# Performance work log

Measured on AMD Instinct MI355X. Metric: run time of the kernel, lower is better.

## Reference

```python
import jax, jax.numpy as jnp
import numpy as np

H = 1024
V = 32000
L = 15
B = 512


def setup_inputs() -> dict:
    key = jax.random.key(0)
    ks = jax.random.split(key, 16)
    s = 0.02
    return {
        "input_ids": jax.random.randint(ks[0], (B,), 0, V),
        "hidden": jax.random.normal(ks[1], (1, B, H), jnp.float32),
        "encoder_outputs": jax.random.normal(ks[2], (L, B, H), jnp.float32),
        "max_length": L,
        "embedding": jax.random.normal(ks[3], (V, H), jnp.float32) * s,
        "attn1_w": jax.random.normal(ks[4], (1, 2 * H), jnp.float32) * s,
        "attn1_b": jnp.zeros((1,), jnp.float32),
        "combine_w": jax.random.normal(ks[5], (H, 2 * H), jnp.float32) * s,
        "combine_b": jnp.zeros((H,), jnp.float32),
        "w_ih": jax.random.normal(ks[6], (3 * H, H), jnp.float32) * s,
        "w_hh": jax.random.normal(ks[7], (3 * H, H), jnp.float32) * s,
        "b_ih": jnp.zeros((3 * H,), jnp.float32),
        "b_hh": jnp.zeros((3 * H,), jnp.float32),
        "out_w": jax.random.normal(ks[8], (V, H), jnp.float32) * s,
        "out_b": jnp.zeros((V,), jnp.float32),
    }


def reference(input_ids, hidden, encoder_outputs, max_length, embedding,
              attn1_w, attn1_b, combine_w, combine_b,
              w_ih, w_hh, b_ih, b_hh, out_w, out_b):
    # embedding lookup (dropout is identity in eval mode)
    emb = embedding[input_ids]                       # [B, H]
    # Bahdanau-style additive scores: vectorize the per-step python loop
    emb_l = jnp.broadcast_to(emb[None], (max_length, B, H))   # [L, B, H]
    cat = jnp.concatenate([emb_l, encoder_outputs], axis=-1)  # [L, B, 2H]
    scores = cat @ attn1_w.T + attn1_b               # [L, B, 1]
    attn_weights = jax.nn.softmax(scores, axis=0)    # softmax over L
    ctx = jnp.sum(attn_weights * encoder_outputs, axis=0)     # [B, H]
    x = jnp.concatenate([emb, ctx], axis=-1) @ combine_w.T + combine_b  # [B, H]
    # n_layers = 1: relu then one GRU step (seq len 1)
    x = jax.nn.relu(x)
    h = hidden[0]                                    # [B, H]
    gi = x @ w_ih.T + b_ih                           # [B, 3H]
    gh = h @ w_hh.T + b_hh                           # [B, 3H]
    i_r, i_z, i_n = jnp.split(gi, 3, axis=1)
    h_r, h_z, h_n = jnp.split(gh, 3, axis=1)
    r = jax.nn.sigmoid(i_r + h_r)
    z = jax.nn.sigmoid(i_z + h_z)
    n = jnp.tanh(i_n + r * h_n)
    h_new = (1.0 - z) * n + z * h                    # [B, H]
    logits = h_new @ out_w.T + out_b                 # [B, V]
    output = jax.nn.log_softmax(logits, axis=1)
    return output, h_new[None], attn_weights
```

## Files before the change

kernel.cpp:

```cpp
#include <hip/hip_runtime.h>

#define HH 1024
#define VV 32000
#define LL 15
#define BB 512

typedef __bf16 bf16;
typedef __bf16 bf16x4 __attribute__((ext_vector_type(4)));
typedef __bf16 bf16x8 __attribute__((ext_vector_type(8)));
typedef float f32x4 __attribute__((ext_vector_type(4)));

#define VMCNT(n) asm volatile("s_waitcnt vmcnt(" #n ")" ::: "memory")
#define LGKM0    asm volatile("s_waitcnt lgkmcnt(0)" ::: "memory")
#define SBAR     __builtin_amdgcn_s_barrier()
#define SCHED0   __builtin_amdgcn_sched_barrier(0)

__device__ __forceinline__ unsigned short f2bf(float f) {
    unsigned int u = __float_as_uint(f);
    unsigned int r = (u + 0x7fffu + ((u >> 16) & 1u)) >> 16;
    return (unsigned short)r;
}

__device__ __forceinline__ void gld_lds16(const void* g, void* l) {
    __builtin_amdgcn_global_load_lds(
        (const __attribute__((address_space(1))) unsigned int*)g,
        (__attribute__((address_space(3))) unsigned int*)l, 16, 0, 0);
}

__global__ __launch_bounds__(256)
void cvt4_kernel(const float* __restrict__ a0, unsigned short* __restrict__ o0, int n0_,
                 const float* __restrict__ a1, unsigned short* __restrict__ o1, int n1_,
                 const float* __restrict__ a2, unsigned short* __restrict__ o2, int n2_,
                 const float* __restrict__ a3, unsigned short* __restrict__ o3, int n3_) {
    int i = blockIdx.x * 256 + threadIdx.x;
    const float* src; unsigned short* dst;
    if (i < n0_) { src = a0; dst = o0; }
    else if ((i -= n0_) < n1_) { src = a1; dst = o1; }
    else if ((i -= n1_) < n2_) { src = a2; dst = o2; }
    else if ((i -= n2_) < n3_) { src = a3; dst = o3; }
    else return;
    const f32x4 a = ((const f32x4*)src)[2 * i], b = ((const f32x4*)src)[2 * i + 1];
    ((bf16x4*)dst)[2 * i]     = __builtin_convertvector(a, bf16x4);
    ((bf16x4*)dst)[2 * i + 1] = __builtin_convertvector(b, bf16x4);
}

__global__ __launch_bounds__(256)
void attn_kernel(const int* __restrict__ ids, const float* __restrict__ enc,
                 const float* __restrict__ embedding,
                 const float* __restrict__ attn1_w, const float* __restrict__ attn1_b,
                 float* __restrict__ attn_out, unsigned short* __restrict__ cat_out) {
    const int b = blockIdx.x, tid = threadIdx.x;
    const int lane = tid & 63, wv = tid >> 6;

    __shared__ float s_enc[LL * HH];
    __shared__ float s_scores[LL];
    __shared__ float s_red[4];

    for (int idx = tid; idx < LL * HH / 4; idx += 256) {
        const int l = (idx * 4) >> 10, h = (idx * 4) & (HH - 1);
        *(f32x4*)&s_enc[idx * 4] = *(const f32x4*)&enc[((size_t)l * BB + b) * HH + h];
    }

    const float* embr = embedding + (size_t)ids[b] * HH;
    float p = 0.f;
    for (int j = tid; j < HH; j += 256) p += embr[j] * attn1_w[j];
    #pragma unroll
    for (int o = 32; o; o >>= 1) p += __shfl_xor(p, o);
    if (lane == 0) s_red[wv] = p;
    __syncthreads();
    const float semb = s_red[0] + s_red[1] + s_red[2] + s_red[3] + attn1_b[0];

    for (int l = wv; l < LL; l += 4) {
        float q = 0.f;
        for (int j = lane; j < HH; j += 64) q += s_enc[l * HH + j] * attn1_w[HH + j];
        #pragma unroll
        for (int o = 32; o; o >>= 1) q += __shfl_xor(q, o);
        if (lane == 0) s_scores[l] = q + semb;
    }
    __syncthreads();

    float mx = -3.4e38f;
    #pragma unroll
    for (int l = 0; l < LL; l++) mx = fmaxf(mx, s_scores[l]);
    float aw[LL], sum = 0.f;
    #pragma unroll
    for (int l = 0; l < LL; l++) { aw[l] = __expf(s_scores[l] - mx); sum += aw[l]; }
    const float inv = 1.f / sum;
    #pragma unroll
    for (int l = 0; l < LL; l++) aw[l] *= inv;

    if (tid < LL) attn_out[tid * BB + b] = aw[tid];

    for (int j = tid; j < HH; j += 256) {
        float c = 0.f;
        #pragma unroll
        for (int l = 0; l < LL; l++) c += aw[l] * s_enc[l * HH + j];
        cat_out[(size_t)b * (2 * HH) + j] = f2bf(embr[j]);
        cat_out[(size_t)b * (2 * HH) + HH + j] = f2bf(c);
    }
}

template<int TM, int TN, int OUT, int GATES>
__global__ __launch_bounds__(256)
void gemm_nt(const bf16* __restrict__ A, const bf16* __restrict__ B,
             const float* __restrict__ bias, void* __restrict__ Cout,
             const bf16* __restrict__ A2, const bf16* __restrict__ B2,
             const float* __restrict__ bias2, void* __restrict__ C2,
             const int K, const int N) {
    constexpr int FM = TM / 32, FN = TN / 32;
    __shared__ bf16 As[2][TM * 64];
    __shared__ bf16 Bs[2][TN * 64];

    if (GATES && blockIdx.z == 1) { A = A2; B = B2; bias = bias2; Cout = C2; }

    const int tid = threadIdx.x;
    const int lane = tid & 63, wave = tid >> 6;
    const int wm = wave >> 1, wn = wave & 1;
    const int rlo = lane & 15, khi = lane >> 4;
    const int m0 = blockIdx.y * TM, n0 = blockIdx.x * TN;

    f32x4 acc[FM][FN] = {};
    constexpr int IA = TM / 32, IB = TN / 32;

    auto stage = [&](int k0, int buf) {
        #pragma unroll
        for (int i = 0; i < IA; i++) {
            const int p = (i * 256 + tid) * 16;
            const int row = p >> 7;
            const int qs = (p & 127) ^ ((row & 7) << 4);
            gld_lds16(A + (size_t)(m0 + row) * K + k0 + (qs >> 1),
                      &As[buf][0] + i * 2048 + wave * 512);
        }
        #pragma unroll
        for (int i = 0; i < IB; i++) {
            const int p = (i * 256 + tid) * 16;
            const int row = p >> 7;
            const int qs = (p & 127) ^ ((row & 7) << 4);
            gld_lds16(B + (size_t)(n0 + row) * K + k0 + (qs >> 1),
                      &Bs[buf][0] + i * 2048 + wave * 512);
        }
    };

    auto compute = [&](int buf) {
        #pragma unroll
        for (int ks = 0; ks < 2; ks++) {
            bf16x8 af[FM], bfr[FN];
            #pragma unroll
            for (int m = 0; m < FM; m++) {
                const int r = wm * (TM / 2) + m * 16 + rlo;
                const int sw = (ks * 64 + khi * 16) ^ ((r & 7) << 4);
                af[m] = *(const bf16x8*)((const char*)&As[buf][0] + r * 128 + sw);
            }
            #pragma unroll
            for (int n = 0; n < FN; n++) {
                const int r = wn * (TN / 2) + n * 16 + rlo;
                const int sw = (ks * 64 + khi * 16) ^ ((r & 7) << 4);
                bfr[n] = *(const bf16x8*)((const char*)&Bs[buf][0] + r * 128 + sw);
            }
            #pragma unroll
            for (int m = 0; m < FM; m++)
                #pragma unroll
                for (int n = 0; n < FN; n++)
                    acc[m][n] = __builtin_amdgcn_mfma_f32_16x16x32_bf16(af[m], bfr[n], acc[m][n], 0, 0, 0);
        }
    };

    const int NT = K >> 6;
    stage(0, 0);
    stage(64, 1);

    for (int kt = 0; kt < NT; kt += 2) {
        {
            const int t = kt;
            if (t + 1 < NT) { VMCNT(4); } else { VMCNT(0); }
            SCHED0; SBAR; SCHED0;
            compute(0);
            SCHED0; SBAR; SCHED0;
            if (t + 2 < NT) stage((t + 2) << 6, 0);
        }
        {
            const int t = kt + 1;
            if (t + 1 < NT) { VMCNT(4); } else { VMCNT(0); }
            SCHED0; SBAR; SCHED0;
            compute(1);
            SCHED0; SBAR; SCHED0;
            if (t + 2 < NT) stage((t + 2) << 6, 1);
        }
    }

    #pragma unroll
    for (int m = 0; m < FM; m++) {
        const int gr = m0 + wm * (TM / 2) + m * 16 + khi * 4;
        #pragma unroll
        for (int n = 0; n < FN; n++) {
            const int gc = n0 + wn * (TN / 2) + n * 16 + rlo;
            const float bv = bias[gc];
            #pragma unroll
            for (int j = 0; j < 4; j++) {
                float v = acc[m][n][j] + bv;
                if (OUT == 1) {
                    v = fmaxf(v, 0.f);
                    ((unsigned short*)Cout)[(size_t)(gr + j) * N + gc] = f2bf(v);
                } else {
                    ((float*)Cout)[(size_t)(gr + j) * N + gc] = v;
                }
            }
        }
    }
}

__global__ __launch_bounds__(256, 3)
void gemm_out(const bf16* __restrict__ A, const float* __restrict__ B,
              const float* __restrict__ bias, float* __restrict__ C,
              float* __restrict__ pmax, float* __restrict__ psum) {
    constexpr int K = HH, N = VV;
    __shared__ bf16 As[2][128 * 64];
    __shared__ bf16 Bs[2][64 * 64];
    __shared__ float sPm[2][128], sPs[2][128];

    const int tid = threadIdx.x;
    const int lane = tid & 63, wave = tid >> 6;
    const int wm = wave >> 1, wn = wave & 1;
    const int rlo = lane & 15, khi = lane >> 4;

    constexpr int gridN = VV / 64;
    constexpr int nFull = (gridN >> 3) << 5;
    const int bidx = blockIdx.x;
    int g, jm;
    if (bidx < nFull) { const int s = bidx >> 5, rem = bidx & 31; jm = rem >> 3; g = s * 8 + (rem & 7); }
    else { const int rem = bidx - nFull; constexpr int gleft = gridN & 7; g = (gridN & ~7) + rem % gleft; jm = rem / gleft; }
    const int n0 = g * 64, m0 = jm * 128;

    f32x4 acc[4][2] = {};
    f32x4 b0[4], b1[4];

    auto loadB = [&](int k0, f32x4* bv) {
        #pragma unroll
        for (int i = 0; i < 4; i++) {
            const int idx = i * 256 + tid;
            const int row = idx >> 4, c4 = idx & 15;
            bv[i] = *(const f32x4*)(B + (size_t)(n0 + row) * K + k0 + c4 * 4);
        }
    };
    auto stageA = [&](int k0, int buf) {
        #pragma unroll
        for (int i = 0; i < 4; i++) {
            const int p = (i * 256 + tid) * 16;
            const int row = p >> 7;
            const int qs = (p & 127) ^ ((row & 7) << 4);
            gld_lds16(A + (size_t)(m0 + row) * K + k0 + (qs >> 1),
                      &As[buf][0] + i * 2048 + wave * 512);
        }
    };
    auto writeB = [&](const f32x4* bv, int buf) {
        #pragma unroll
        for (int i = 0; i < 4; i++) {
            const int idx = i * 256 + tid;
            const int row = idx >> 4, c4 = idx & 15;
            bf16x4 w = __builtin_convertvector(bv[i], bf16x4);
            *(bf16x4*)((char*)&Bs[buf][0] + row * 128 + ((c4 * 8) ^ ((row & 7) << 4))) = w;
        }
    };
    auto compute = [&](int buf) {
        #pragma unroll
        for (int ks = 0; ks < 2; ks++) {
            bf16x8 af[4], bfr[2];
            #pragma unroll
            for (int m = 0; m < 4; m++) {
                const int r = wm * 64 + m * 16 + rlo;
                const int sw = (ks * 64 + khi * 16) ^ ((r & 7) << 4);
                af[m] = *(const bf16x8*)((const char*)&As[buf][0] + r * 128 + sw);
            }
            #pragma unroll
            for (int n = 0; n < 2; n++) {
                const int r = wn * 32 + n * 16 + rlo;
                const int sw = (ks * 64 + khi * 16) ^ ((r & 7) << 4);
                bfr[n] = *(const bf16x8*)((const char*)&Bs[buf][0] + r * 128 + sw);
            }
            #pragma unroll
            for (int m = 0; m < 4; m++)
                #pragma unroll
                for (int n = 0; n < 2; n++)
                    acc[m][n] = __builtin_amdgcn_mfma_f32_16x16x32_bf16(af[m], bfr[n], acc[m][n], 0, 0, 0);
        }
    };

    constexpr int NT = K >> 6;
    loadB(0, b0);
    stageA(0, 0);
    VMCNT(4);
    writeB(b0, 0);
    loadB(64, b1);
    stageA(64, 1);

    for (int kt = 0; kt < NT; kt += 2) {
        {
            const int t = kt;
            if (t + 1 < NT) { VMCNT(8); } else { VMCNT(0); }
            LGKM0;
            SCHED0; SBAR; SCHED0;
            compute(0);
            SCHED0; SBAR; SCHED0;
            if (t + 1 < NT) { VMCNT(4); writeB(b1, 1); }
            if (t + 2 < NT) { loadB((t + 2) << 6, b0); stageA((t + 2) << 6, 0); }
        }
        {
            const int t = kt + 1;
            if (t + 1 < NT) { VMCNT(8); } else { VMCNT(0); }
            LGKM0;
            SCHED0; SBAR; SCHED0;
            compute(1);
            SCHED0; SBAR; SCHED0;
            if (t + 1 < NT) { VMCNT(4); writeB(b0, 0); }
            if (t + 2 < NT) { loadB((t + 2) << 6, b1); stageA((t + 2) << 6, 1); }
        }
    }

    float bvn[2];
    #pragma unroll
    for (int n = 0; n < 2; n++) bvn[n] = bias[n0 + wn * 32 + n * 16 + rlo];

    #pragma unroll
    for (int m = 0; m < 4; m++) {
        const int rbase = wm * 64 + m * 16 + khi * 4;
        #pragma unroll
        for (int j = 0; j < 4; j++) {
            const int gr = m0 + rbase + j;
            float v[2];
            #pragma unroll
            for (int n = 0; n < 2; n++) {
                v[n] = acc[m][n][j] + bvn[n];
                C[(size_t)gr * N + n0 + wn * 32 + n * 16 + rlo] = v[n];
            }
            float lm = fmaxf(v[0], v[1]);
            #pragma unroll
            for (int o = 8; o; o >>= 1) lm = fmaxf(lm, __shfl_xor(lm, o));
            float ls = __expf(v[0] - lm) + __expf(v[1] - lm);
            #pragma unroll
            for (int o = 8; o; o >>= 1) ls += __shfl_xor(ls, o);
            if (rlo == 0) { sPm[wn][rbase + j] = lm; sPs[wn][rbase + j] = ls; }
        }
    }
    __syncthreads();
    if (tid < 128) {
        const float ma = sPm[0][tid], mb = sPm[1][tid];
        const float M = fmaxf(ma, mb);
        const float S = sPs[0][tid] * __expf(ma - M) + sPs[1][tid] * __expf(mb - M);
        pmax[(size_t)(m0 + tid) * 512 + g] = M;
        psum[(size_t)(m0 + tid) * 512 + g] = S;
    }
}

__global__ __launch_bounds__(256)
void gru_kernel(const float* __restrict__ gi, const float* __restrict__ gh,
                const float* __restrict__ h, float* __restrict__ hnew,
                unsigned short* __restrict__ hnew_bf) {
    const int i = blockIdx.x * 256 + threadIdx.x;
    const int e = i * 4;
    const int b = e >> 10, j = e & (HH - 1);
    const size_t o = ((size_t)b * 3 * HH + j) / 4;
    const f32x4 ir = ((const f32x4*)gi)[o],          iz = ((const f32x4*)gi)[o + HH / 4],
                in_ = ((const f32x4*)gi)[o + 2 * HH / 4];
    const f32x4 hr = ((const f32x4*)gh)[o],          hz = ((const f32x4*)gh)[o + HH / 4],
                hn = ((const f32x4*)gh)[o + 2 * HH / 4];
    const f32x4 hv = ((const f32x4*)h)[i];
    f32x4 out;
    ushort4 ob;
    #pragma unroll
    for (int c = 0; c < 4; c++) {
        const float r = 1.f / (1.f + __expf(-(ir[c] + hr[c])));
        const float z = 1.f / (1.f + __expf(-(iz[c] + hz[c])));
        const float n = tanhf(in_[c] + r * hn[c]);
        const float v = (1.f - z) * n + z * hv[c];
        out[c] = v;
        ((unsigned short*)&ob)[c] = f2bf(v);
    }
    ((f32x4*)hnew)[i] = out;
    ((ushort4*)hnew_bf)[i] = ob;
}

__global__ __launch_bounds__(512)
void lsm_final(const float* __restrict__ pmax, const float* __restrict__ psum,
               float* __restrict__ logits) {
    const int b = blockIdx.x, tid = threadIdx.x;
    const int lane = tid & 63, wv = tid >> 6;
    __shared__ float sm[8], ss[8];

    float m = -3.4e38f, s = 0.f;
    if (tid < VV / 64) { m = pmax[(size_t)b * 512 + tid]; s = psum[(size_t)b * 512 + tid]; }
    #pragma unroll
    for (int o = 32; o; o >>= 1) {
        const float mo = __shfl_xor(m, o), so = __shfl_xor(s, o);
        const float nm = fmaxf(m, mo);
        s = s * __expf(m - nm) + so * __expf(mo - nm);
        m = nm;
    }
    if (lane == 0) { sm[wv] = m; ss[wv] = s; }
    __syncthreads();
    float M = sm[0], S;
    #pragma unroll
    for (int w = 1; w < 8; w++) M = fmaxf(M, sm[w]);
    S = ss[0] * __expf(sm[0] - M);
    #pragma unroll
    for (int w = 1; w < 8; w++) S += ss[w] * __expf(sm[w] - M);
    const float lse = M + __logf(S);

    float* row = logits + (size_t)b * VV;
    for (int j = tid; j < VV / 4; j += 512) {
        f32x4 v = ((const f32x4*)row)[j];
        v[0] -= lse; v[1] -= lse; v[2] -= lse; v[3] -= lse;
        ((f32x4*)row)[j] = v;
    }
}

extern "C" void kernel_launch(void* const* d_in, const int* in_sizes, int n_in,
                              void* d_out, int out_size, void* d_ws, size_t ws_size,
                              hipStream_t stream) {
    const int*   ids       = (const int*)d_in[0];
    const float* hidden    = (const float*)d_in[1];
    const float* enc       = (const float*)d_in[2];
    const float* embedding = (const float*)d_in[4];
    const float* attn1_w   = (const float*)d_in[5];
    const float* attn1_b   = (const float*)d_in[6];
    const float* combine_w = (const float*)d_in[7];
    const float* combine_b = (const float*)d_in[8];
    const float* w_ih      = (const float*)d_in[9];
    const float* w_hh      = (const float*)d_in[10];
    const float* b_ih      = (const float*)d_in[11];
    const float* b_hh      = (const float*)d_in[12];
    const float* out_w     = (const float*)d_in[13];
    const float* out_b     = (const float*)d_in[14];

    float* out_lsm = (float*)d_out;
    float* out_h   = out_lsm + (size_t)BB * VV;
    float* out_aw  = out_h + (size_t)BB * HH;

    char* w = (char*)d_ws;
    unsigned short* w_ih_bf  = (unsigned short*)w;   w += (size_t)3 * HH * HH * 2;
    unsigned short* w_hh_bf  = (unsigned short*)w;   w += (size_t)3 * HH * HH * 2;
    unsigned short* w_cb_bf  = (unsigned short*)w;   w += (size_t)2 * HH * HH * 2;
    unsigned short* cat_bf   = (unsigned short*)w;   w += (size_t)BB * 2 * HH * 2;
    unsigned short* x_bf     = (unsigned short*)w;   w += (size_t)BB * HH * 2;
    unsigned short* hid_bf   = (unsigned short*)w;   w += (size_t)BB * HH * 2;
    unsigned short* hnew_bf  = (unsigned short*)w;   w += (size_t)BB * HH * 2;
    float* gi   = (float*)w;                         w += (size_t)BB * 3 * HH * 4;
    float* gh   = (float*)w;                         w += (size_t)BB * 3 * HH * 4;
    float* pmax = (float*)w;                         w += (size_t)BB * 512 * 4;
    float* psum = (float*)w;                         w += (size_t)BB * 512 * 4;

    cvt4_kernel<<<(3 * HH * HH / 8 * 2 + 2 * HH * HH / 8 + BB * HH / 8) / 256, 256, 0, stream>>>(
        w_ih, w_ih_bf, 3 * HH * HH / 8,
        w_hh, w_hh_bf, 3 * HH * HH / 8,
        combine_w, w_cb_bf, 2 * HH * HH / 8,
        hidden, hid_bf, BB * HH / 8);

    attn_kernel<<<BB, 256, 0, stream>>>(ids, enc, embedding, attn1_w, attn1_b, out_aw, cat_bf);

    gemm_nt<64, 64, 1, 0><<<dim3(HH / 64, BB / 64), 256, 0, stream>>>(
        (const bf16*)cat_bf, (const bf16*)w_cb_bf, combine_b, x_bf,
        nullptr, nullptr, nullptr, nullptr, 2 * HH, HH);

    gemm_nt<64, 64, 0, 1><<<dim3(3 * HH / 64, BB / 64, 2), 256, 0, stream>>>(
        (const bf16*)hid_bf, (const bf16*)w_hh_bf, b_hh, gh,
        (const bf16*)x_bf, (const bf16*)w_ih_bf, b_ih, gi, HH, 3 * HH);

    gru_kernel<<<(BB * HH / 4) / 256, 256, 0, stream>>>(gi, gh, hidden, out_h, hnew_bf);

    gemm_out<<<(VV / 64) * 4, 256, 0, stream>>>(
        (const bf16*)hnew_bf, out_w, out_b, out_lsm, pmax, psum);

    lsm_final<<<BB, 512, 0, stream>>>(pmax, psum, out_lsm);
}
```

Measured before the change: 182.7 us.

## Pre-pack output weights to tiled bf16 and stream them via direct-to-LDS loads

Adds a pack kernel that converts out_w from fp32 to bf16 in a tile-contiguous layout (64 rows x 64 k per 8KB chunk), then changes gemm_out to load B with global_load_lds directly into shared memory instead of going through registers with fp32 loads and conversion. The vocabulary is processed in two halves so the packed buffer holds only 16000 rows, adding two extra launches and a write-then-read of the packed weights each call. The aim is to cut VGPR traffic and the LDS write/convert step in the main loop, at the cost of an extra pass over out_w.

```diff
diff --git a/kernel.cpp b/kernel.cpp
--- a/kernel.cpp
+++ b/kernel.cpp
@@ -11,7 +11,6 @@
 typedef float f32x4 __attribute__((ext_vector_type(4)));
 
 #define VMCNT(n) asm volatile("s_waitcnt vmcnt(" #n ")" ::: "memory")
-#define LGKM0    asm volatile("s_waitcnt lgkmcnt(0)" ::: "memory")
 #define SBAR     __builtin_amdgcn_s_barrier()
 #define SCHED0   __builtin_amdgcn_sched_barrier(0)
 
@@ -45,6 +44,23 @@
 }
 
 __global__ __launch_bounds__(256)
+void pack_w(const float* __restrict__ src, unsigned short* __restrict__ dst) {
+    const int b = blockIdx.x;
+    const int g = b >> 2, q = b & 3;
+    const float* pan = src + (size_t)g * 65536;
+    char* pd = (char*)(dst + (size_t)g * 65536);
+    #pragma unroll
+    for (int j = 0; j < 16; j++) {
+        const int s4 = q * 4096 + j * 256 + threadIdx.x;
+        const f32x4 v = ((const f32x4*)pan)[s4];
+        const int sp = s4 * 4;
+        const int r = sp >> 10, k = sp & 1023;
+        bf16x4 w = __builtin_convertvector(v, bf16x4);
+        *(bf16x4*)(pd + ((k >> 6) << 13) + (r << 7) + ((k & 63) << 1)) = w;
+    }
+}
+
+__global__ __launch_bounds__(256)
 void attn_kernel(const int* __restrict__ ids, const float* __restrict__ enc,
                  const float* __restrict__ embedding,
                  const float* __restrict__ attn1_w, const float* __restrict__ attn1_b,
@@ -210,9 +226,9 @@
 }
 
 __global__ __launch_bounds__(256, 3)
-void gemm_out(const bf16* __restrict__ A, const float* __restrict__ B,
+void gemm_out(const bf16* __restrict__ A, const bf16* __restrict__ Bp,
               const float* __restrict__ bias, float* __restrict__ C,
-              float* __restrict__ pmax, float* __restrict__ psum) {
+              float* __restrict__ pmax, float* __restrict__ psum, const int nbase) {
     constexpr int K = HH, N = VV;
     __shared__ bf16 As[2][128 * 64];
     __shared__ bf16 Bs[2][64 * 64];
@@ -223,26 +239,19 @@
     const int wm = wave >> 1, wn = wave & 1;
     const int rlo = lane & 15, khi = lane >> 4;
 
-    constexpr int gridN = VV / 64;
+    constexpr int gridN = 250;
     constexpr int nFull = (gridN >> 3) << 5;
     const int bidx = blockIdx.x;
     int g, jm;
     if (bidx < nFull) { const int s = bidx >> 5, rem = bidx & 31; jm = rem >> 3; g = s * 8 + (rem & 7); }
     else { const int rem = bidx - nFull; constexpr int gleft = gridN & 7; g = (gridN & ~7) + rem % gleft; jm = rem / gleft; }
-    const int n0 = g * 64, m0 = jm * 128;
+    const int n0 = nbase + g * 64, m0 = jm * 128;
+
+    const char* tile_base = (const char*)Bp + (size_t)g * 131072;
 
     f32x4 acc[4][2] = {};
-    f32x4 b0[4], b1[4];
-
-    auto loadB = [&](int k0, f32x4* bv) {
-        #pragma unroll
-        for (int i = 0; i < 4; i++) {
-            const int idx = i * 256 + tid;
-            const int row = idx >> 4, c4 = idx & 15;
-            bv[i] = *(const f32x4*)(B + (size_t)(n0 + row) * K + k0 + c4 * 4);
-        }
-    };
-    auto stageA = [&](int k0, int buf) {
+
+    auto stage = [&](int k0, int buf) {
         #pragma unroll
         for (int i = 0; i < 4; i++) {
             const int p = (i * 256 + tid) * 16;
@@ -251,16 +260,16 @@
             gld_lds16(A + (size_t)(m0 + row) * K + k0 + (qs >> 1),
                       &As[buf][0] + i * 2048 + wave * 512);
         }
+        #pragma unroll
+        for (int i = 0; i < 2; i++) {
+            const int p = (i * 256 + tid) * 16;
+            const int row = p >> 7;
+            const int qs = (p & 127) ^ ((row & 7) << 4);
+            gld_lds16(tile_base + (size_t)k0 * 128 + row * 128 + qs,
+                      &Bs[buf][0] + i * 2048 + wave * 512);
+        }
     };
-    auto writeB = [&](const f32x4* bv, int buf) {
-        #pragma unroll
-        for (int i = 0; i < 4; i++) {
-            const int idx = i * 256 + tid;
-            const int row = idx >> 4, c4 = idx & 15;
-            bf16x4 w = __builtin_convertvector(bv[i], bf16x4);
-            *(bf16x4*)((char*)&Bs[buf][0] + row * 128 + ((c4 * 8) ^ ((row & 7) << 4))) = w;
-        }
-    };
+
     auto compute = [&](int buf) {
         #pragma unroll
         for (int ks = 0; ks < 2; ks++) {
@@ -286,33 +295,25 @@
     };
 
     constexpr int NT = K >> 6;
-    loadB(0, b0);
-    stageA(0, 0);
-    VMCNT(4);
-    writeB(b0, 0);
-    loadB(64, b1);
-    stageA(64, 1);
+    stage(0, 0);
+    stage(64, 1);
 
     for (int kt = 0; kt < NT; kt += 2) {
         {
             const int t = kt;
-            if (t + 1 < NT) { VMCNT(8); } else { VMCNT(0); }
-            LGKM0;
+            if (t + 1 < NT) { VMCNT(6); } else { VMCNT(0); }
             SCHED0; SBAR; SCHED0;
             compute(0);
             SCHED0; SBAR; SCHED0;
-            if (t + 1 < NT) { VMCNT(4); writeB(b1, 1); }
-            if (t + 2 < NT) { loadB((t + 2) << 6, b0); stageA((t + 2) << 6, 0); }
+            if (t + 2 < NT) stage((t + 2) << 6, 0);
         }
         {
             const int t = kt + 1;
-            if (t + 1 < NT) { VMCNT(8); } else { VMCNT(0); }
-            LGKM0;
+            if (t + 1 < NT) { VMCNT(6); } else { VMCNT(0); }
             SCHED0; SBAR; SCHED0;
             compute(1);
             SCHED0; SBAR; SCHED0;
-            if (t + 1 < NT) { VMCNT(4); writeB(b0, 0); }
-            if (t + 2 < NT) { loadB((t + 2) << 6, b1); stageA((t + 2) << 6, 1); }
+            if (t + 2 < NT) stage((t + 2) << 6, 1);
         }
     }
 
@@ -346,8 +347,9 @@
         const float ma = sPm[0][tid], mb = sPm[1][tid];
         const float M = fmaxf(ma, mb);
         const float S = sPs[0][tid] * __expf(ma - M) + sPs[1][tid] * __expf(mb - M);
-        pmax[(size_t)(m0 + tid) * 512 + g] = M;
-        psum[(size_t)(m0 + tid) * 512 + g] = S;
+        const int gg = (nbase >> 6) + g;
+        pmax[(size_t)(m0 + tid) * 512 + gg] = M;
+        psum[(size_t)(m0 + tid) * 512 + gg] = S;
     }
 }
 
@@ -447,6 +449,7 @@
     float* gh   = (float*)w;                         w += (size_t)BB * 3 * HH * 4;
     float* pmax = (float*)w;                         w += (size_t)BB * 512 * 4;
     float* psum = (float*)w;                         w += (size_t)BB * 512 * 4;
+    unsigned short* packed = (unsigned short*)w;     w += (size_t)16000 * HH * 2;
 
     cvt4_kernel<<<(3 * HH * HH / 8 * 2 + 2 * HH * HH / 8 + BB * HH / 8) / 256, 256, 0, stream>>>(
         w_ih, w_ih_bf, 3 * HH * HH / 8,
@@ -466,8 +469,13 @@
 
     gru_kernel<<<(BB * HH / 4) / 256, 256, 0, stream>>>(gi, gh, hidden, out_h, hnew_bf);
 
-    gemm_out<<<(VV / 64) * 4, 256, 0, stream>>>(
-        (const bf16*)hnew_bf, out_w, out_b, out_lsm, pmax, psum);
+    pack_w<<<1000, 256, 0, stream>>>(out_w, packed);
+    gemm_out<<<1000, 256, 0, stream>>>(
+        (const bf16*)hnew_bf, (const bf16*)packed, out_b, out_lsm, pmax, psum, 0);
+
+    pack_w<<<1000, 256, 0, stream>>>(out_w + (size_t)16000 * HH, packed);
+    gemm_out<<<1000, 256, 0, stream>>>(
+        (const bf16*)hnew_bf, (const bf16*)packed, out_b, out_lsm, pmax, psum, 16000);
 
     lsm_final<<<BB, 512, 0, stream>>>(pmax, psum, out_lsm);
 }
```

New measurement: 208.6 us. 14.2% more time.

## Load output-GEMM operands directly to registers, dropping LDS staging

Applied to the files above, without the earlier changes.

The vocab-projection GEMM no longer stages A and B tiles through double-buffered LDS with barriers. Each wave now loads its MFMA fragments straight from global memory, converting the fp32 weights to bf16 in registers. The cross-wave partial softmax merge through shared memory is also removed, with each wave writing its own (max, sum) pair, which doubles the partial buffer that lsm_final reduces. This removes LDS traffic and synchronisation, but data reuse now depends on caches, loads are uncoalesced per-lane row accesses, and register pressure rises, so occupancy is lowered to 2 blocks.

```diff
diff --git a/kernel.cpp b/kernel.cpp
--- a/kernel.cpp
+++ b/kernel.cpp
@@ -11,7 +11,6 @@
 typedef float f32x4 __attribute__((ext_vector_type(4)));
 
 #define VMCNT(n) asm volatile("s_waitcnt vmcnt(" #n ")" ::: "memory")
-#define LGKM0    asm volatile("s_waitcnt lgkmcnt(0)" ::: "memory")
 #define SBAR     __builtin_amdgcn_s_barrier()
 #define SCHED0   __builtin_amdgcn_sched_barrier(0)
 
@@ -209,15 +208,11 @@
     }
 }
 
-__global__ __launch_bounds__(256, 3)
+__global__ __launch_bounds__(256, 2)
 void gemm_out(const bf16* __restrict__ A, const float* __restrict__ B,
               const float* __restrict__ bias, float* __restrict__ C,
               float* __restrict__ pmax, float* __restrict__ psum) {
     constexpr int K = HH, N = VV;
-    __shared__ bf16 As[2][128 * 64];
-    __shared__ bf16 Bs[2][64 * 64];
-    __shared__ float sPm[2][128], sPs[2][128];
-
     const int tid = threadIdx.x;
     const int lane = tid & 63, wave = tid >> 6;
     const int wm = wave >> 1, wn = wave & 1;
@@ -232,100 +227,53 @@
     const int n0 = g * 64, m0 = jm * 128;
 
     f32x4 acc[4][2] = {};
-    f32x4 b0[4], b1[4];
-
-    auto loadB = [&](int k0, f32x4* bv) {
-        #pragma unroll
-        for (int i = 0; i < 4; i++) {
-            const int idx = i * 256 + tid;
-            const int row = idx >> 4, c4 = idx & 15;
-            bv[i] = *(const f32x4*)(B + (size_t)(n0 + row) * K + k0 + c4 * 4);
-        }
-    };
-    auto stageA = [&](int k0, int buf) {
-        #pragma unroll
-        for (int i = 0; i < 4; i++) {
-            const int p = (i * 256 + tid) * 16;
-            const int row = p >> 7;
-            const int qs = (p & 127) ^ ((row & 7) << 4);
-            gld_lds16(A + (size_t)(m0 + row) * K + k0 + (qs >> 1),
-                      &As[buf][0] + i * 2048 + wave * 512);
-        }
-    };
-    auto writeB = [&](const f32x4* bv, int buf) {
-        #pragma unroll
-        for (int i = 0; i < 4; i++) {
-            const int idx = i * 256 + tid;
-            const int row = idx >> 4, c4 = idx & 15;
-            bf16x4 w = __builtin_convertvector(bv[i], bf16x4);
-            *(bf16x4*)((char*)&Bs[buf][0] + row * 128 + ((c4 * 8) ^ ((row & 7) << 4))) = w;
-        }
-    };
-    auto compute = [&](int buf) {
-        #pragma unroll
-        for (int ks = 0; ks < 2; ks++) {
-            bf16x8 af[4], bfr[2];
-            #pragma unroll
-            for (int m = 0; m < 4; m++) {
-                const int r = wm * 64 + m * 16 + rlo;
-                const int sw = (ks * 64 + khi * 16) ^ ((r & 7) << 4);
-                af[m] = *(const bf16x8*)((const char*)&As[buf][0] + r * 128 + sw);
-            }
-            #pragma unroll
-            for (int n = 0; n < 2; n++) {
-                const int r = wn * 32 + n * 16 + rlo;
-                const int sw = (ks * 64 + khi * 16) ^ ((r & 7) << 4);
-                bfr[n] = *(const bf16x8*)((const char*)&Bs[buf][0] + r * 128 + sw);
-            }
+
+    const bf16*  Abase = A + (size_t)(m0 + wm * 64 + rlo) * K + khi * 8;
+    const float* Bbase = B + (size_t)(n0 + wn * 32 + rlo) * K + khi * 8;
+
+    #pragma unroll 4
+    for (int kt = 0; kt < 16; kt++) {
+        const int k0 = kt * 64;
+        bf16x8 af[4][2];
+        #pragma unroll
+        for (int m = 0; m < 4; m++)
+            #pragma unroll
+            for (int ks = 0; ks < 2; ks++)
+                af[m][ks] = *(const bf16x8*)(Abase + (size_t)m * 16 * K + k0 + ks * 32);
+        bf16x8 bfr[2][2];
+        #pragma unroll
+        for (int n = 0; n < 2; n++)
+            #pragma unroll
+            for (int ks = 0; ks < 2; ks++) {
+                const float* p = Bbase + (size_t)n * 16 * K + k0 + ks * 32;
+                const f32x4 lo = *(const f32x4*)p;
+                const f32x4 hi = *(const f32x4*)(p + 4);
+                const bf16x4 a = __builtin_convertvector(lo, bf16x4);
+                const bf16x4 b = __builtin_convertvector(hi, bf16x4);
+                bf16x8 r;
+                #pragma unroll
+                for (int c = 0; c < 4; c++) { r[c] = a[c]; r[c + 4] = b[c]; }
+                bfr[n][ks] = r;
+            }
+        #pragma unroll
+        for (int ks = 0; ks < 2; ks++)
             #pragma unroll
             for (int m = 0; m < 4; m++)
                 #pragma unroll
                 for (int n = 0; n < 2; n++)
-                    acc[m][n] = __builtin_amdgcn_mfma_f32_16x16x32_bf16(af[m], bfr[n], acc[m][n], 0, 0, 0);
-        }
-    };
-
-    constexpr int NT = K >> 6;
-    loadB(0, b0);
-    stageA(0, 0);
-    VMCNT(4);
-    writeB(b0, 0);
-    loadB(64, b1);
-    stageA(64, 1);
-
-    for (int kt = 0; kt < NT; kt += 2) {
-        {
-            const int t = kt;
-            if (t + 1 < NT) { VMCNT(8); } else { VMCNT(0); }
-            LGKM0;
-            SCHED0; SBAR; SCHED0;
-            compute(0);
-            SCHED0; SBAR; SCHED0;
-            if (t + 1 < NT) { VMCNT(4); writeB(b1, 1); }
-            if (t + 2 < NT) { loadB((t + 2) << 6, b0); stageA((t + 2) << 6, 0); }
-        }
-        {
-            const int t = kt + 1;
-            if (t + 1 < NT) { VMCNT(8); } else { VMCNT(0); }
-            LGKM0;
-            SCHED0; SBAR; SCHED0;
-            compute(1);
-            SCHED0; SBAR; SCHED0;
-            if (t + 1 < NT) { VMCNT(4); writeB(b0, 0); }
-            if (t + 2 < NT) { loadB((t + 2) << 6, b1); stageA((t + 2) << 6, 1); }
-        }
+                    acc[m][n] = __builtin_amdgcn_mfma_f32_16x16x32_bf16(af[m][ks], bfr[n][ks], acc[m][n], 0, 0, 0);
     }
 
     float bvn[2];
     #pragma unroll
     for (int n = 0; n < 2; n++) bvn[n] = bias[n0 + wn * 32 + n * 16 + rlo];
 
+    const int pcol = g * 2 + wn;
     #pragma unroll
     for (int m = 0; m < 4; m++) {
-        const int rbase = wm * 64 + m * 16 + khi * 4;
         #pragma unroll
         for (int j = 0; j < 4; j++) {
-            const int gr = m0 + rbase + j;
+            const int gr = m0 + wm * 64 + m * 16 + khi * 4 + j;
             float v[2];
             #pragma unroll
             for (int n = 0; n < 2; n++) {
@@ -338,16 +286,11 @@
             float ls = __expf(v[0] - lm) + __expf(v[1] - lm);
             #pragma unroll
             for (int o = 8; o; o >>= 1) ls += __shfl_xor(ls, o);
-            if (rlo == 0) { sPm[wn][rbase + j] = lm; sPs[wn][rbase + j] = ls; }
-        }
-    }
-    __syncthreads();
-    if (tid < 128) {
-        const float ma = sPm[0][tid], mb = sPm[1][tid];
-        const float M = fmaxf(ma, mb);
-        const float S = sPs[0][tid] * __expf(ma - M) + sPs[1][tid] * __expf(mb - M);
-        pmax[(size_t)(m0 + tid) * 512 + g] = M;
-        psum[(size_t)(m0 + tid) * 512 + g] = S;
+            if (rlo == 0) {
+                pmax[(size_t)gr * 1024 + pcol] = lm;
+                psum[(size_t)gr * 1024 + pcol] = ls;
+            }
+        }
     }
 }
 
@@ -387,7 +330,12 @@
     __shared__ float sm[8], ss[8];
 
     float m = -3.4e38f, s = 0.f;
-    if (tid < VV / 64) { m = pmax[(size_t)b * 512 + tid]; s = psum[(size_t)b * 512 + tid]; }
+    for (int j = tid; j < 1000; j += 512) {
+        const float mo = pmax[(size_t)b * 1024 + j], so = psum[(size_t)b * 1024 + j];
+        const float nm = fmaxf(m, mo);
+        s = s * __expf(m - nm) + so * __expf(mo - nm);
+        m = nm;
+    }
     #pragma unroll
     for (int o = 32; o; o >>= 1) {
         const float mo = __shfl_xor(m, o), so = __shfl_xor(s, o);
@@ -445,8 +393,8 @@
     unsigned short* hnew_bf  = (unsigned short*)w;   w += (size_t)BB * HH * 2;
     float* gi   = (float*)w;                         w += (size_t)BB * 3 * HH * 4;
     float* gh   = (float*)w;                         w += (size_t)BB * 3 * HH * 4;
-    float* pmax = (float*)w;                         w += (size_t)BB * 512 * 4;
-    float* psum = (float*)w;                         w += (size_t)BB * 512 * 4;
+    float* pmax = (float*)w;                         w += (size_t)BB * 1024 * 4;
+    float* psum = (float*)w;                         w += (size_t)BB * 1024 * 4;
 
     cvt4_kernel<<<(3 * HH * HH / 8 * 2 + 2 * HH * HH / 8 + BB * HH / 8) / 256, 256, 0, stream>>>(
         w_ih, w_ih_bf, 3 * HH * HH / 8,
```

New measurement: 370.0 us. +102.6%, slower.
